# Optimization experiments

Hardware: AMD Instinct MI355X
Metric: run time of the kernel (lower is better)

Reference implementation:

```python
import jax, jax.numpy as jnp
import numpy as np

NUM_HEADS = 8
WINDOW = 8


def setup_inputs() -> dict:
    key = jax.random.key(0)
    k1, k2, k3, k4 = jax.random.split(key, 4)
    B, H, W, C = 8, 192, 192, 192
    x = jax.random.normal(k1, (B, H * W, C), dtype=jnp.float32)
    w_qkv = jax.random.normal(k2, (C, 3 * C), dtype=jnp.float32) * 0.02
    w_proj = jax.random.normal(k3, (C, C), dtype=jnp.float32) * 0.02
    b_proj = jax.random.normal(k4, (C,), dtype=jnp.float32) * 0.02
    return {"x": x, "w_qkv": w_qkv, "w_proj": w_proj, "b_proj": b_proj, "H": H, "W": W}


def reference(x, w_qkv, w_proj, b_proj, H, W):
    B, L, C = x.shape
    N = WINDOW * WINDOW  # 64 tokens per window
    Nw = L // N          # number of windows (torch view chain == flat reshape, no permute)
    scale = (C // NUM_HEADS) ** -0.5
    # qkv projection on flat tokens, then window reshape
    qkv = (x @ w_qkv).reshape(B, Nw, N, 3, C)
    q = qkv[..., 0, :]
    k = qkv[..., 1, :] * scale
    v = qkv[..., 2, :]
    # channel attention: [B,Nw,C,C]
    attn = jnp.einsum('bwnc,bwnd->bwcd', k, v)
    attn = jax.nn.softmax(attn, axis=-1)
    # out[b,w,n,c] = sum_d attn[b,w,c,d] * q[b,w,n,d]
    out = jnp.einsum('bwcd,bwnd->bwnc', attn, q)
    out = out.reshape(B, L, C)
    return out @ w_proj + b_proj
```

## Files before the change

kernel.cpp:

```cpp
#include <hip/hip_runtime.h>
#include <hip/hip_bf16.h>

typedef short bf16x8 __attribute__((ext_vector_type(8)));
typedef float f32x4  __attribute__((ext_vector_type(4)));

__device__ __forceinline__ unsigned short f2bf(float f) {
  unsigned int u = __float_as_uint(f);
  u += 0x7fffu + ((u >> 16) & 1u);
  return (unsigned short)(u >> 16);
}

__device__ __forceinline__ f32x4 fzero() { f32x4 z = {0.f, 0.f, 0.f, 0.f}; return z; }

#define WQKV_FRAGS (6*36*64)
#define WP_FRAGS   (6*12*64)
#define WQKV_ELEMS (WQKV_FRAGS*8)

__global__ void prepack_weights(const float* __restrict__ wqkv,
                                const float* __restrict__ wproj,
                                unsigned short* __restrict__ ws) {
  int t = blockIdx.x * 256 + threadIdx.x;
  const float scale = 0.20412414523193154f;
  if (t < WQKV_FRAGS) {
    int kt  = t / (36*64);
    int rem = t - kt*(36*64);
    int nt  = rem >> 6;
    int l   = rem & 63;
    int n   = nt*16 + (l & 15);
    int k0  = kt*32 + (l >> 4)*8;
    float s = (n >= 192 && n < 384) ? scale : 1.0f;
    union { unsigned short us[8]; uint4 v; } u;
#pragma unroll
    for (int j = 0; j < 8; ++j) u.us[j] = f2bf(wqkv[(k0 + j)*576 + n] * s);
    *(uint4*)(ws + (size_t)t * 8) = u.v;
  } else if (t < WQKV_FRAGS + WP_FRAGS) {
    int t2  = t - WQKV_FRAGS;
    int kt  = t2 / (12*64);
    int rem = t2 - kt*(12*64);
    int nt  = rem >> 6;
    int l   = rem & 63;
    int n   = nt*16 + (l & 15);
    int k0  = kt*32 + (l >> 4)*8;
    union { unsigned short us[8]; uint4 v; } u;
#pragma unroll
    for (int j = 0; j < 8; ++j) u.us[j] = f2bf(wproj[(k0 + j)*192 + n]);
    *(uint4*)(ws + (size_t)WQKV_ELEMS + (size_t)t2 * 8) = u.v;
  }
}

__launch_bounds__(768, 3)
__global__ void win_attn_fused(const float* __restrict__ x,
                               const unsigned short* __restrict__ wqkv_sw,
                               const unsigned short* __restrict__ wp_sw,
                               const float* __restrict__ bias,
                               float* __restrict__ out) {
  __shared__ __align__(16) unsigned char smem[117248];
  unsigned short* sX   = (unsigned short*)(smem);
  unsigned short* sP   = (unsigned short*)(smem);
  unsigned short* sQ   = (unsigned short*)(smem + 25600);
  unsigned short* sKt  = (unsigned short*)(smem + 51200);
  unsigned short* sVt  = (unsigned short*)(smem + 78848);
  unsigned short* sOut = (unsigned short*)(smem + 106496);
  float2*         sRed = (float2*)(smem + 115712);

  const int tid  = threadIdx.x;
  const int lane = tid & 63;
  const int wv   = tid >> 6;
  const int l16  = lane & 15;
  const int lq   = lane >> 4;

  {
    const float4* xg = (const float4*)(x + (size_t)blockIdx.x * 12288);
#pragma unroll
    for (int i = 0; i < 4; ++i) {
      int idx = tid + i * 768;
      float4 v = xg[idx];
      int e = idx << 2;
      unsigned short* p = sX + (e / 192) * 200 + (e % 192);
      p[0] = f2bf(v.x); p[1] = f2bf(v.y); p[2] = f2bf(v.z); p[3] = f2bf(v.w);
    }
  }
  __syncthreads();

  {
    bf16x8 af[4][6];
#pragma unroll
    for (int ms = 0; ms < 4; ++ms)
#pragma unroll
      for (int kt = 0; kt < 6; ++kt)
        af[ms][kt] = *(const bf16x8*)(sX + (ms*16 + l16)*200 + kt*32 + lq*8);

    for (int nt = wv; nt < 36; nt += 12) {
      f32x4 acc[4] = {fzero(), fzero(), fzero(), fzero()};
      const bf16x8* bp = (const bf16x8*)wqkv_sw + nt*64 + lane;
#pragma unroll
      for (int kt = 0; kt < 6; ++kt) {
        bf16x8 b = bp[kt * (36*64)];
#pragma unroll
        for (int ms = 0; ms < 4; ++ms)
          acc[ms] = __builtin_amdgcn_mfma_f32_16x16x32_bf16(af[ms][kt], b, acc[ms], 0, 0, 0);
      }
      int c = nt*16 + l16;
#pragma unroll
      for (int ms = 0; ms < 4; ++ms) {
        int rb = ms*16 + lq*4;
        if (c < 192) {
#pragma unroll
          for (int r = 0; r < 4; ++r) sQ[(rb + r)*200 + c] = f2bf(acc[ms][r]);
        } else if (c < 384) {
#pragma unroll
          for (int r = 0; r < 4; ++r) sKt[(c - 192)*72 + rb + r] = f2bf(acc[ms][r]);
        } else {
#pragma unroll
          for (int r = 0; r < 4; ++r) sVt[(c - 384)*72 + rb + r] = f2bf(acc[ms][r]);
        }
      }
    }
  }
  __syncthreads();

  f32x4 accF[4];
#pragma unroll
  for (int m = 0; m < 4; ++m) accF[m] = fzero();

  const int ccs = wv & 3;
  const int thr = wv >> 2;

  bf16x8 av[4][2];
#pragma unroll
  for (int mi = 0; mi < 4; ++mi)
#pragma unroll
    for (int kt = 0; kt < 2; ++kt) {
      int rd = thr*64 + mi*16 + l16;
      av[mi][kt] = *(const bf16x8*)(sVt + rd*72 + kt*32 + lq*8);
    }

  const int ct = wv & 3, mh = wv >> 2;
  bf16x8 aq[2][6];
  if (wv < 8) {
#pragma unroll
    for (int mi = 0; mi < 2; ++mi)
#pragma unroll
      for (int kt = 0; kt < 6; ++kt)
        aq[mi][kt] = *(const bf16x8*)(sQ + ((mh*2 + mi)*16 + l16)*200 + kt*32 + lq*8);
  }

  for (int cb = 0; cb < 3; ++cb) {
    f32x4 lac[4] = {fzero(), fzero(), fzero(), fzero()};
    {
      int rc = cb*64 + ccs*16 + l16;
#pragma unroll
      for (int kt = 0; kt < 2; ++kt) {
        bf16x8 b = *(const bf16x8*)(sKt + rc*72 + kt*32 + lq*8);
#pragma unroll
        for (int mi = 0; mi < 4; ++mi)
          lac[mi] = __builtin_amdgcn_mfma_f32_16x16x32_bf16(av[mi][kt], b, lac[mi], 0, 0, 0);
      }
    }

    int ccl = ccs*16 + l16;
    {
      float l[16];
#pragma unroll
      for (int mi = 0; mi < 4; ++mi)
#pragma unroll
        for (int r = 0; r < 4; ++r) l[mi*4+r] = lac[mi][r];
      float mx = l[0];
#pragma unroll
      for (int i = 1; i < 16; ++i) mx = fmaxf(mx, l[i]);
      mx = fmaxf(mx, __shfl_xor(mx, 16));
      mx = fmaxf(mx, __shfl_xor(mx, 32));
      float s = 0.f;
#pragma unroll
      for (int i = 0; i < 16; ++i) { float e = __expf(l[i] - mx); l[i] = e; s += e; }
      s += __shfl_xor(s, 16);
      s += __shfl_xor(s, 32);
      if (lane < 16) sRed[thr*64 + ccl] = make_float2(mx, s);
      __syncthreads();
      float2 r0 = sRed[ccl], r1 = sRed[64 + ccl], r2 = sRed[128 + ccl];
      float M = fmaxf(fmaxf(r0.x, r1.x), r2.x);
      float S = r0.y*__expf(r0.x - M) + r1.y*__expf(r1.x - M) + r2.y*__expf(r2.x - M);
      float sc = __expf(mx - M) / S;
#pragma unroll
      for (int mi = 0; mi < 4; ++mi) {
        int d0 = thr*64 + mi*16 + lq*4;
        union { unsigned short us[4]; uint2 v; } u;
        u.us[0] = f2bf(l[mi*4+0]*sc); u.us[1] = f2bf(l[mi*4+1]*sc);
        u.us[2] = f2bf(l[mi*4+2]*sc); u.us[3] = f2bf(l[mi*4+3]*sc);
        *(uint2*)(sP + ccl*200 + d0) = u.v;
      }
    }
    __syncthreads();

    if (wv < 8) {
      f32x4 acc[2] = {fzero(), fzero()};
#pragma unroll
      for (int kt = 0; kt < 6; ++kt) {
        bf16x8 b = *(const bf16x8*)(sP + (ct*16 + l16)*200 + kt*32 + lq*8);
#pragma unroll
        for (int mi = 0; mi < 2; ++mi)
          acc[mi] = __builtin_amdgcn_mfma_f32_16x16x32_bf16(aq[mi][kt], b, acc[mi], 0, 0, 0);
      }
#pragma unroll
      for (int mi = 0; mi < 2; ++mi)
#pragma unroll
        for (int r = 0; r < 4; ++r)
          sOut[((mh*2 + mi)*16 + lq*4 + r)*72 + ct*16 + l16] = f2bf(acc[mi][r]);
    }
    __syncthreads();

    {
      bf16x8 ao[4][2];
#pragma unroll
      for (int ms = 0; ms < 4; ++ms)
#pragma unroll
        for (int kt = 0; kt < 2; ++kt)
          ao[ms][kt] = *(const bf16x8*)(sOut + (ms*16 + l16)*72 + kt*32 + lq*8);
      const bf16x8* bp = (const bf16x8*)wp_sw + ((cb*2)*12 + wv)*64 + lane;
#pragma unroll
      for (int kt = 0; kt < 2; ++kt) {
        bf16x8 b = bp[kt * (12*64)];
#pragma unroll
        for (int ms = 0; ms < 4; ++ms)
          accF[ms] = __builtin_amdgcn_mfma_f32_16x16x32_bf16(ao[ms][kt], b, accF[ms], 0, 0, 0);
      }
    }
  }

  {
    int e = wv*16 + l16;
    float bv = bias[e];
    float* op = out + (size_t)blockIdx.x * 12288;
#pragma unroll
    for (int ms = 0; ms < 4; ++ms)
#pragma unroll
      for (int r = 0; r < 4; ++r)
        op[(ms*16 + lq*4 + r)*192 + e] = accF[ms][r] + bv;
  }
}

extern "C" void kernel_launch(void* const* d_in, const int* in_sizes, int n_in,
                              void* d_out, int out_size, void* d_ws, size_t ws_size,
                              hipStream_t stream) {
  const float* x     = (const float*)d_in[0];
  const float* wqkv  = (const float*)d_in[1];
  const float* wproj = (const float*)d_in[2];
  const float* bproj = (const float*)d_in[3];
  unsigned short* ws = (unsigned short*)d_ws;

  int nwin = in_sizes[0] / 12288;

  prepack_weights<<<72, 256, 0, stream>>>(wqkv, wproj, ws);
  win_attn_fused<<<nwin, 768, 0, stream>>>(x, ws, ws + WQKV_ELEMS, bproj, (float*)d_out);
}
```

Baseline: 518.4 us.

## Widen fused window-attention block to 16 waves and redistribute per-wave tiles

Raises the block from 768 to 1024 threads (16 waves) and reassigns work across the QKV GEMM, the channel-attention logits and softmax, the P·Q product and the output projection. Each wave now owns one 16-row m-tile and a strided set of n-tiles, and the softmax reduction spans four row groups of 48. The aim is more resident waves per CU for latency hiding, with all 16 waves busy in the P·Q stage instead of 8. The cost is fewer m-tiles per weight fragment, so each block issues roughly four times as many global/L2 weight loads. There is also a tighter per-thread register budget and a slightly larger shared reduction buffer.

```diff
diff --git a/kernel.cpp b/kernel.cpp
--- a/kernel.cpp
+++ b/kernel.cpp
@@ -48,13 +48,13 @@
   }
 }
 
-__launch_bounds__(768, 3)
+__launch_bounds__(1024, 4)
 __global__ void win_attn_fused(const float* __restrict__ x,
                                const unsigned short* __restrict__ wqkv_sw,
                                const unsigned short* __restrict__ wp_sw,
                                const float* __restrict__ bias,
                                float* __restrict__ out) {
-  __shared__ __align__(16) unsigned char smem[117248];
+  __shared__ __align__(16) unsigned char smem[117760];
   unsigned short* sX   = (unsigned short*)(smem);
   unsigned short* sP   = (unsigned short*)(smem);
   unsigned short* sQ   = (unsigned short*)(smem + 25600);
@@ -72,8 +72,8 @@
   {
     const float4* xg = (const float4*)(x + (size_t)blockIdx.x * 12288);
 #pragma unroll
-    for (int i = 0; i < 4; ++i) {
-      int idx = tid + i * 768;
+    for (int i = 0; i < 3; ++i) {
+      int idx = tid + i * 1024;
       float4 v = xg[idx];
       int e = idx << 2;
       unsigned short* p = sX + (e / 192) * 200 + (e % 192);
@@ -83,107 +83,98 @@
   __syncthreads();
 
   {
-    bf16x8 af[4][6];
-#pragma unroll
-    for (int ms = 0; ms < 4; ++ms)
+    const int ms1 = wv & 3;
+    const int ng1 = wv >> 2;
+    bf16x8 af[6];
+#pragma unroll
+    for (int kt = 0; kt < 6; ++kt)
+      af[kt] = *(const bf16x8*)(sX + (ms1*16 + l16)*200 + kt*32 + lq*8);
+
+#pragma unroll
+    for (int k = 0; k < 9; ++k) {
+      int nt = ng1 + 4*k;
+      f32x4 acc = fzero();
+      const bf16x8* bp = (const bf16x8*)wqkv_sw + nt*64 + lane;
 #pragma unroll
       for (int kt = 0; kt < 6; ++kt)
-        af[ms][kt] = *(const bf16x8*)(sX + (ms*16 + l16)*200 + kt*32 + lq*8);
-
-    for (int nt = wv; nt < 36; nt += 12) {
-      f32x4 acc[4] = {fzero(), fzero(), fzero(), fzero()};
-      const bf16x8* bp = (const bf16x8*)wqkv_sw + nt*64 + lane;
-#pragma unroll
-      for (int kt = 0; kt < 6; ++kt) {
-        bf16x8 b = bp[kt * (36*64)];
-#pragma unroll
-        for (int ms = 0; ms < 4; ++ms)
-          acc[ms] = __builtin_amdgcn_mfma_f32_16x16x32_bf16(af[ms][kt], b, acc[ms], 0, 0, 0);
-      }
-      int c = nt*16 + l16;
-#pragma unroll
-      for (int ms = 0; ms < 4; ++ms) {
-        int rb = ms*16 + lq*4;
-        if (c < 192) {
-#pragma unroll
-          for (int r = 0; r < 4; ++r) sQ[(rb + r)*200 + c] = f2bf(acc[ms][r]);
-        } else if (c < 384) {
-#pragma unroll
-          for (int r = 0; r < 4; ++r) sKt[(c - 192)*72 + rb + r] = f2bf(acc[ms][r]);
-        } else {
-#pragma unroll
-          for (int r = 0; r < 4; ++r) sVt[(c - 384)*72 + rb + r] = f2bf(acc[ms][r]);
-        }
+        acc = __builtin_amdgcn_mfma_f32_16x16x32_bf16(af[kt], bp[kt * (36*64)], acc, 0, 0, 0);
+      int c  = nt*16 + l16;
+      int rb = ms1*16 + lq*4;
+      if (c < 192) {
+#pragma unroll
+        for (int r = 0; r < 4; ++r) sQ[(rb + r)*200 + c] = f2bf(acc[r]);
+      } else if (c < 384) {
+#pragma unroll
+        for (int r = 0; r < 4; ++r) sKt[(c - 192)*72 + rb + r] = f2bf(acc[r]);
+      } else {
+#pragma unroll
+        for (int r = 0; r < 4; ++r) sVt[(c - 384)*72 + rb + r] = f2bf(acc[r]);
       }
     }
   }
   __syncthreads();
-
-  f32x4 accF[4];
-#pragma unroll
-  for (int m = 0; m < 4; ++m) accF[m] = fzero();
 
   const int ccs = wv & 3;
   const int thr = wv >> 2;
 
-  bf16x8 av[4][2];
-#pragma unroll
-  for (int mi = 0; mi < 4; ++mi)
+  bf16x8 av[3][2];
+#pragma unroll
+  for (int mi = 0; mi < 3; ++mi)
 #pragma unroll
     for (int kt = 0; kt < 2; ++kt) {
-      int rd = thr*64 + mi*16 + l16;
+      int rd = thr*48 + mi*16 + l16;
       av[mi][kt] = *(const bf16x8*)(sVt + rd*72 + kt*32 + lq*8);
     }
 
-  const int ct = wv & 3, mh = wv >> 2;
-  bf16x8 aq[2][6];
-  if (wv < 8) {
-#pragma unroll
-    for (int mi = 0; mi < 2; ++mi)
-#pragma unroll
-      for (int kt = 0; kt < 6; ++kt)
-        aq[mi][kt] = *(const bf16x8*)(sQ + ((mh*2 + mi)*16 + l16)*200 + kt*32 + lq*8);
-  }
+  bf16x8 aq[6];
+#pragma unroll
+  for (int kt = 0; kt < 6; ++kt)
+    aq[kt] = *(const bf16x8*)(sQ + ((wv & 3)*16 + l16)*200 + kt*32 + lq*8);
+
+  f32x4 accF[3];
+#pragma unroll
+  for (int m = 0; m < 3; ++m) accF[m] = fzero();
 
   for (int cb = 0; cb < 3; ++cb) {
-    f32x4 lac[4] = {fzero(), fzero(), fzero(), fzero()};
+    f32x4 lac[3] = {fzero(), fzero(), fzero()};
     {
       int rc = cb*64 + ccs*16 + l16;
 #pragma unroll
       for (int kt = 0; kt < 2; ++kt) {
         bf16x8 b = *(const bf16x8*)(sKt + rc*72 + kt*32 + lq*8);
 #pragma unroll
-        for (int mi = 0; mi < 4; ++mi)
+        for (int mi = 0; mi < 3; ++mi)
           lac[mi] = __builtin_amdgcn_mfma_f32_16x16x32_bf16(av[mi][kt], b, lac[mi], 0, 0, 0);
       }
     }
 
     int ccl = ccs*16 + l16;
     {
-      float l[16];
-#pragma unroll
-      for (int mi = 0; mi < 4; ++mi)
+      float l[12];
+#pragma unroll
+      for (int mi = 0; mi < 3; ++mi)
 #pragma unroll
         for (int r = 0; r < 4; ++r) l[mi*4+r] = lac[mi][r];
       float mx = l[0];
 #pragma unroll
-      for (int i = 1; i < 16; ++i) mx = fmaxf(mx, l[i]);
+      for (int i = 1; i < 12; ++i) mx = fmaxf(mx, l[i]);
       mx = fmaxf(mx, __shfl_xor(mx, 16));
       mx = fmaxf(mx, __shfl_xor(mx, 32));
       float s = 0.f;
 #pragma unroll
-      for (int i = 0; i < 16; ++i) { float e = __expf(l[i] - mx); l[i] = e; s += e; }
+      for (int i = 0; i < 12; ++i) { float e = __expf(l[i] - mx); l[i] = e; s += e; }
       s += __shfl_xor(s, 16);
       s += __shfl_xor(s, 32);
       if (lane < 16) sRed[thr*64 + ccl] = make_float2(mx, s);
       __syncthreads();
-      float2 r0 = sRed[ccl], r1 = sRed[64 + ccl], r2 = sRed[128 + ccl];
-      float M = fmaxf(fmaxf(r0.x, r1.x), r2.x);
-      float S = r0.y*__expf(r0.x - M) + r1.y*__expf(r1.x - M) + r2.y*__expf(r2.x - M);
+      float2 r0 = sRed[ccl], r1 = sRed[64 + ccl], r2 = sRed[128 + ccl], r3 = sRed[192 + ccl];
+      float M = fmaxf(fmaxf(r0.x, r1.x), fmaxf(r2.x, r3.x));
+      float S = r0.y*__expf(r0.x - M) + r1.y*__expf(r1.x - M)
+              + r2.y*__expf(r2.x - M) + r3.y*__expf(r3.x - M);
       float sc = __expf(mx - M) / S;
 #pragma unroll
-      for (int mi = 0; mi < 4; ++mi) {
-        int d0 = thr*64 + mi*16 + lq*4;
+      for (int mi = 0; mi < 3; ++mi) {
+        int d0 = thr*48 + mi*16 + lq*4;
         union { unsigned short us[4]; uint2 v; } u;
         u.us[0] = f2bf(l[mi*4+0]*sc); u.us[1] = f2bf(l[mi*4+1]*sc);
         u.us[2] = f2bf(l[mi*4+2]*sc); u.us[3] = f2bf(l[mi*4+3]*sc);
@@ -192,50 +183,48 @@
     }
     __syncthreads();
 
-    if (wv < 8) {
-      f32x4 acc[2] = {fzero(), fzero()};
+    {
+      int ct3 = wv >> 2;
+      f32x4 acc = fzero();
 #pragma unroll
       for (int kt = 0; kt < 6; ++kt) {
-        bf16x8 b = *(const bf16x8*)(sP + (ct*16 + l16)*200 + kt*32 + lq*8);
-#pragma unroll
-        for (int mi = 0; mi < 2; ++mi)
-          acc[mi] = __builtin_amdgcn_mfma_f32_16x16x32_bf16(aq[mi][kt], b, acc[mi], 0, 0, 0);
-      }
-#pragma unroll
-      for (int mi = 0; mi < 2; ++mi)
-#pragma unroll
-        for (int r = 0; r < 4; ++r)
-          sOut[((mh*2 + mi)*16 + lq*4 + r)*72 + ct*16 + l16] = f2bf(acc[mi][r]);
+        bf16x8 b = *(const bf16x8*)(sP + (ct3*16 + l16)*200 + kt*32 + lq*8);
+        acc = __builtin_amdgcn_mfma_f32_16x16x32_bf16(aq[kt], b, acc, 0, 0, 0);
+      }
+#pragma unroll
+      for (int r = 0; r < 4; ++r)
+        sOut[((wv & 3)*16 + lq*4 + r)*72 + ct3*16 + l16] = f2bf(acc[r]);
     }
     __syncthreads();
 
     {
-      bf16x8 ao[4][2];
-#pragma unroll
-      for (int ms = 0; ms < 4; ++ms)
-#pragma unroll
-        for (int kt = 0; kt < 2; ++kt)
-          ao[ms][kt] = *(const bf16x8*)(sOut + (ms*16 + l16)*72 + kt*32 + lq*8);
-      const bf16x8* bp = (const bf16x8*)wp_sw + ((cb*2)*12 + wv)*64 + lane;
-#pragma unroll
-      for (int kt = 0; kt < 2; ++kt) {
-        bf16x8 b = bp[kt * (12*64)];
-#pragma unroll
-        for (int ms = 0; ms < 4; ++ms)
-          accF[ms] = __builtin_amdgcn_mfma_f32_16x16x32_bf16(ao[ms][kt], b, accF[ms], 0, 0, 0);
+      bf16x8 ao[2];
+#pragma unroll
+      for (int kt = 0; kt < 2; ++kt)
+        ao[kt] = *(const bf16x8*)(sOut + ((wv & 3)*16 + l16)*72 + kt*32 + lq*8);
+#pragma unroll
+      for (int k = 0; k < 3; ++k) {
+        int nt = (wv >> 2) + 4*k;
+#pragma unroll
+        for (int kt = 0; kt < 2; ++kt) {
+          bf16x8 b = *((const bf16x8*)wp_sw + (((cb*2 + kt)*12) + nt)*64 + lane);
+          accF[k] = __builtin_amdgcn_mfma_f32_16x16x32_bf16(ao[kt], b, accF[k], 0, 0, 0);
+        }
       }
     }
   }
 
   {
-    int e = wv*16 + l16;
-    float bv = bias[e];
     float* op = out + (size_t)blockIdx.x * 12288;
 #pragma unroll
-    for (int ms = 0; ms < 4; ++ms)
+    for (int k = 0; k < 3; ++k) {
+      int nt = (wv >> 2) + 4*k;
+      int e  = nt*16 + l16;
+      float bv = bias[e];
 #pragma unroll
       for (int r = 0; r < 4; ++r)
-        op[(ms*16 + lq*4 + r)*192 + e] = accF[ms][r] + bv;
+        op[((wv & 3)*16 + lq*4 + r)*192 + e] = accF[k][r] + bv;
+    }
   }
 }
 
@@ -251,5 +240,5 @@
   int nwin = in_sizes[0] / 12288;
 
   prepack_weights<<<72, 256, 0, stream>>>(wqkv, wproj, ws);
-  win_attn_fused<<<nwin, 768, 0, stream>>>(x, ws, ws + WQKV_ELEMS, bproj, (float*)d_out);
-}
+  win_attn_fused<<<nwin, 1024, 0, stream>>>(x, ws, ws + WQKV_ELEMS, bproj, (float*)d_out);
+}
```

Result: slower. 582.6 us (+12.4%).
